# Optimization experiments

Measured on AMD Instinct MI355X. Metric: run time of the kernel, lower is better.

Reference implementation:

```python
import jax, jax.numpy as jnp
import numpy as np

INV_SQRT2 = 0.7071067811865476  # Haar (db1) lowpass on a length-1 zero-padded signal: cA = x/sqrt(2)


def setup_inputs() -> dict:
    key = jax.random.key(0)
    k = jax.random.split(key, 6)
    batch, node, dim = 4, 512, 64
    x = jax.random.normal(k[0], (batch, node, dim), dtype=jnp.float32)
    w0 = jax.random.normal(k[1], (1, 1), dtype=jnp.float32)   # linear[0].weight (always index 0 in source)
    b0 = jax.random.normal(k[2], (1,), dtype=jnp.float32)     # linear[0].bias
    wa = jax.random.normal(k[3], (dim,), dtype=jnp.float32)   # stacked attn_fc[i].weight (each 1x1)
    ba = jax.random.normal(k[4], (dim,), dtype=jnp.float32)   # stacked attn_fc[i].bias
    adj = jax.random.randint(k[5], (node, node), 0, 2, dtype=jnp.int32)
    return {"x": x, "w0": w0, "b0": b0, "wa": wa, "ba": ba, "adj": adj}


def reference(x, w0, b0, wa, ba, adj):
    # x: (b, n, d). Per-channel wavelet feature: softplus(linear0(cA)), cA = x/sqrt(2).
    feat = jax.nn.softplus(x * (INV_SQRT2 * w0[0, 0]) + b0[0])          # (b, n, d)
    scores = feat * wa + ba                                              # (b, n, d): attn_fc[i] per channel
    mask = adj > 0                                                       # (n, n)
    # attn_matrix[b,i,j,d] = scores[b,j,d] * mask[i,j], then masked-fill -1e9 where mask==0
    logits = scores[:, None, :, :] * mask[None, :, :, None].astype(scores.dtype)
    logits = jnp.where(mask[None, :, :, None], logits, jnp.float32(-1e9))
    attn = jax.nn.softmax(logits, axis=2)                                # softmax over j (neighbors)
    out = jnp.einsum('bijd,bjd->bid', attn, feat)                        # (b, n, d)
    return out
```

## Files before the change

kernel.cpp:

```cpp
#include <hip/hip_runtime.h>

#define NODE 512
#define DIM 64
#define BATCH 4

typedef __attribute__((ext_vector_type(8))) short bf16x8;
typedef __attribute__((ext_vector_type(4))) float f32x4;

#define LSTRIDE 520

__device__ __forceinline__ unsigned short f2bf(float f) {
    unsigned int u = __float_as_uint(f);
    u += 0x7FFF + ((u >> 16) & 1);
    return (unsigned short)(u >> 16);
}

__global__ __launch_bounds__(512) void k_fused3(const float* __restrict__ x,
                                                const float* __restrict__ w0,
                                                const float* __restrict__ b0,
                                                const float* __restrict__ wa,
                                                const float* __restrict__ ba,
                                                const int* __restrict__ adj,
                                                float* __restrict__ out) {
    __shared__ unsigned short Ep[16][LSTRIDE];
    __shared__ unsigned short Wp[16][LSTRIDE];
    __shared__ f32x4 red[2][4][2][64];

    const int blk = blockIdx.x;
    const int dt  = blk & 3;
    const int itg = (blk >> 2) & 15;
    const int b   = blk >> 6;
    const int tid = threadIdx.x;
    const int i0  = itg * 32;
    const int d0  = dt * 16;

    const int lane = tid & 63;
    const int w    = tid >> 6;
    const int itl  = w & 1;
    const int kq   = w >> 1;
    const int fr   = lane & 15;
    const int kg   = lane >> 4;

    const int* pAdj = adj + (i0 + itl * 16 + fr) * NODE + kq * 128 + kg * 8;
    int4 pa0[4], pa1[4];
    #pragma unroll
    for (int m = 0; m < 4; ++m) {
        pa0[m] = *(const int4*)(pAdj + m * 32);
        pa1[m] = *(const int4*)(pAdj + m * 32 + 4);
    }

    {
        const float c  = 0.7071067811865476f * w0[0];
        const float bb = b0[0];
        #pragma unroll
        for (int iter = 0; iter < 2; ++iter) {
            const int task = iter * 512 + tid;
            const int dg = task & 3;
            const int jp = task >> 2;
            const float* px = x + ((size_t)(b * NODE + 2 * jp) * DIM) + d0 + dg * 4;
            const float4 x0 = *(const float4*)px;
            const float4 x1 = *(const float4*)(px + DIM);
            #pragma unroll
            for (int i = 0; i < 4; ++i) {
                const int dl = dg * 4 + i;
                const float xv0 = (i == 0) ? x0.x : (i == 1) ? x0.y : (i == 2) ? x0.z : x0.w;
                const float xv1 = (i == 0) ? x1.x : (i == 1) ? x1.y : (i == 2) ? x1.z : x1.w;
                const float wad = wa[d0 + dl], bad = ba[d0 + dl];
                float z0 = fmaf(xv0, c, bb), z1 = fmaf(xv1, c, bb);
                float f0 = fmaxf(z0, 0.f) + __logf(1.f + __expf(-fabsf(z0)));
                float f1 = fmaxf(z1, 0.f) + __logf(1.f + __expf(-fabsf(z1)));
                float e0 = __expf(fmaf(f0, wad, bad));
                float e1 = __expf(fmaf(f1, wad, bad));
                unsigned int epk = (unsigned int)f2bf(e0) | ((unsigned int)f2bf(e1) << 16);
                unsigned int wpk = (unsigned int)f2bf(e0 * f0) | ((unsigned int)f2bf(e1 * f1) << 16);
                *(unsigned int*)&Ep[dl][2 * jp] = epk;
                *(unsigned int*)&Wp[dl][2 * jp] = wpk;
            }
        }
    }
    __syncthreads();

    const int jb0 = kq * 128 + kg * 8;
    f32x4 accD = {0.f, 0.f, 0.f, 0.f};
    f32x4 accN = {0.f, 0.f, 0.f, 0.f};
    #pragma unroll
    for (int m = 0; m < 4; ++m) {
        union { bf16x8 v; unsigned short s[8]; } A;
        A.s[0] = pa0[m].x ? 0x3F80 : 0;  A.s[1] = pa0[m].y ? 0x3F80 : 0;
        A.s[2] = pa0[m].z ? 0x3F80 : 0;  A.s[3] = pa0[m].w ? 0x3F80 : 0;
        A.s[4] = pa1[m].x ? 0x3F80 : 0;  A.s[5] = pa1[m].y ? 0x3F80 : 0;
        A.s[6] = pa1[m].z ? 0x3F80 : 0;  A.s[7] = pa1[m].w ? 0x3F80 : 0;
        const int jb = jb0 + m * 32;
        bf16x8 BD = *(const bf16x8*)&Ep[fr][jb];
        bf16x8 BN = *(const bf16x8*)&Wp[fr][jb];
        accD = __builtin_amdgcn_mfma_f32_16x16x32_bf16(A.v, BD, accD, 0, 0, 0);
        accN = __builtin_amdgcn_mfma_f32_16x16x32_bf16(A.v, BN, accN, 0, 0, 0);
    }

    red[itl][kq][0][lane] = accD;
    red[itl][kq][1][lane] = accN;
    __syncthreads();

    if (w < 2) {
        const int t = w;
        f32x4 D = red[t][0][0][lane] + red[t][1][0][lane] + red[t][2][0][lane] + red[t][3][0][lane];
        f32x4 N = red[t][0][1][lane] + red[t][1][1][lane] + red[t][2][1][lane] + red[t][3][1][lane];
        #pragma unroll
        for (int r = 0; r < 4; ++r) {
            float dd = D[r], nn = N[r];
            float o = (dd != 0.f) ? nn / dd : 0.f;
            out[((b * NODE) + i0 + t * 16 + kg * 4 + r) * DIM + d0 + fr] = o;
        }
    }
}

extern "C" void kernel_launch(void* const* d_in, const int* in_sizes, int n_in,
                              void* d_out, int out_size, void* d_ws, size_t ws_size,
                              hipStream_t stream) {
    const float* x  = (const float*)d_in[0];
    const float* w0 = (const float*)d_in[1];
    const float* b0 = (const float*)d_in[2];
    const float* wa = (const float*)d_in[3];
    const float* ba = (const float*)d_in[4];
    const int*  adj = (const int*)d_in[5];
    float* out = (float*)d_out;

    k_fused3<<<dim3(256), dim3(512), 0, stream>>>(x, w0, b0, wa, ba, adj, out);
}
```

Before: 9.895 us.

## Halve rows per block to 16 and split K over 8 waves, doubling grid

Each block now handles 16 output rows instead of 32, with all 8 waves splitting the 512-neighbor dimension into 64-wide chunks, and the grid grows from 256 to 512 blocks. This spreads work across more CUs on the GPU and shortens each wave's adjacency load and MFMA chain. All x loads are also issued up front before the softplus/exp work. The cost is that every block recomputes the full 512x16 exp/feature tables, so total transcendental work doubles, and the final reduction sums 8 partials in a single wave.

Result: slower. 10.86 us (+9.8%).

```diff
diff --git a/kernel.cpp b/kernel.cpp
--- a/kernel.cpp
+++ b/kernel.cpp
@@ -15,7 +15,7 @@
     return (unsigned short)(u >> 16);
 }
 
-__global__ __launch_bounds__(512) void k_fused3(const float* __restrict__ x,
+__global__ __launch_bounds__(512) void k_fused4(const float* __restrict__ x,
                                                 const float* __restrict__ w0,
                                                 const float* __restrict__ b0,
                                                 const float* __restrict__ wa,
@@ -24,47 +24,54 @@
                                                 float* __restrict__ out) {
     __shared__ unsigned short Ep[16][LSTRIDE];
     __shared__ unsigned short Wp[16][LSTRIDE];
-    __shared__ f32x4 red[2][4][2][64];
+    __shared__ f32x4 red[8][2][64];
 
     const int blk = blockIdx.x;
     const int dt  = blk & 3;
-    const int itg = (blk >> 2) & 15;
-    const int b   = blk >> 6;
+    const int it  = (blk >> 2) & 31;
+    const int b   = blk >> 7;
     const int tid = threadIdx.x;
-    const int i0  = itg * 32;
+    const int i0  = it * 16;
     const int d0  = dt * 16;
 
     const int lane = tid & 63;
     const int w    = tid >> 6;
-    const int itl  = w & 1;
-    const int kq   = w >> 1;
     const int fr   = lane & 15;
     const int kg   = lane >> 4;
 
-    const int* pAdj = adj + (i0 + itl * 16 + fr) * NODE + kq * 128 + kg * 8;
-    int4 pa0[4], pa1[4];
+    const int* pAdj = adj + (i0 + fr) * NODE + w * 64 + kg * 8;
+    int4 pa0[2], pa1[2];
     #pragma unroll
-    for (int m = 0; m < 4; ++m) {
+    for (int m = 0; m < 2; ++m) {
         pa0[m] = *(const int4*)(pAdj + m * 32);
         pa1[m] = *(const int4*)(pAdj + m * 32 + 4);
     }
 
     {
+        const int task0 = tid;
+        const int task1 = 512 + tid;
+        const int dgA = task0 & 3, jpA = task0 >> 2;
+        const int dgB = task1 & 3, jpB = task1 >> 2;
+        const float* pxA = x + ((size_t)(b * NODE + 2 * jpA) * DIM) + d0 + dgA * 4;
+        const float* pxB = x + ((size_t)(b * NODE + 2 * jpB) * DIM) + d0 + dgB * 4;
+        const float4 xA0 = *(const float4*)pxA;
+        const float4 xA1 = *(const float4*)(pxA + DIM);
+        const float4 xB0 = *(const float4*)pxB;
+        const float4 xB1 = *(const float4*)(pxB + DIM);
         const float c  = 0.7071067811865476f * w0[0];
         const float bb = b0[0];
+
         #pragma unroll
-        for (int iter = 0; iter < 2; ++iter) {
-            const int task = iter * 512 + tid;
-            const int dg = task & 3;
-            const int jp = task >> 2;
-            const float* px = x + ((size_t)(b * NODE + 2 * jp) * DIM) + d0 + dg * 4;
-            const float4 x0 = *(const float4*)px;
-            const float4 x1 = *(const float4*)(px + DIM);
+        for (int hh = 0; hh < 2; ++hh) {
+            const int dg = hh ? dgB : dgA;
+            const int jp = hh ? jpB : jpA;
+            const float4 v0 = hh ? xB0 : xA0;
+            const float4 v1 = hh ? xB1 : xA1;
             #pragma unroll
             for (int i = 0; i < 4; ++i) {
                 const int dl = dg * 4 + i;
-                const float xv0 = (i == 0) ? x0.x : (i == 1) ? x0.y : (i == 2) ? x0.z : x0.w;
-                const float xv1 = (i == 0) ? x1.x : (i == 1) ? x1.y : (i == 2) ? x1.z : x1.w;
+                const float xv0 = (i == 0) ? v0.x : (i == 1) ? v0.y : (i == 2) ? v0.z : v0.w;
+                const float xv1 = (i == 0) ? v1.x : (i == 1) ? v1.y : (i == 2) ? v1.z : v1.w;
                 const float wad = wa[d0 + dl], bad = ba[d0 + dl];
                 float z0 = fmaf(xv0, c, bb), z1 = fmaf(xv1, c, bb);
                 float f0 = fmaxf(z0, 0.f) + __logf(1.f + __expf(-fabsf(z0)));
@@ -80,11 +87,11 @@
     }
     __syncthreads();
 
-    const int jb0 = kq * 128 + kg * 8;
+    const int jb0 = w * 64 + kg * 8;
     f32x4 accD = {0.f, 0.f, 0.f, 0.f};
     f32x4 accN = {0.f, 0.f, 0.f, 0.f};
     #pragma unroll
-    for (int m = 0; m < 4; ++m) {
+    for (int m = 0; m < 2; ++m) {
         union { bf16x8 v; unsigned short s[8]; } A;
         A.s[0] = pa0[m].x ? 0x3F80 : 0;  A.s[1] = pa0[m].y ? 0x3F80 : 0;
         A.s[2] = pa0[m].z ? 0x3F80 : 0;  A.s[3] = pa0[m].w ? 0x3F80 : 0;
@@ -97,19 +104,23 @@
         accN = __builtin_amdgcn_mfma_f32_16x16x32_bf16(A.v, BN, accN, 0, 0, 0);
     }
 
-    red[itl][kq][0][lane] = accD;
-    red[itl][kq][1][lane] = accN;
+    red[w][0][lane] = accD;
+    red[w][1][lane] = accN;
     __syncthreads();
 
-    if (w < 2) {
-        const int t = w;
-        f32x4 D = red[t][0][0][lane] + red[t][1][0][lane] + red[t][2][0][lane] + red[t][3][0][lane];
-        f32x4 N = red[t][0][1][lane] + red[t][1][1][lane] + red[t][2][1][lane] + red[t][3][1][lane];
+    if (w == 0) {
+        f32x4 D = red[0][0][lane];
+        f32x4 N = red[0][1][lane];
+        #pragma unroll
+        for (int q = 1; q < 8; ++q) {
+            D += red[q][0][lane];
+            N += red[q][1][lane];
+        }
         #pragma unroll
         for (int r = 0; r < 4; ++r) {
             float dd = D[r], nn = N[r];
             float o = (dd != 0.f) ? nn / dd : 0.f;
-            out[((b * NODE) + i0 + t * 16 + kg * 4 + r) * DIM + d0 + fr] = o;
+            out[((b * NODE) + i0 + kg * 4 + r) * DIM + d0 + fr] = o;
         }
     }
 }
@@ -125,5 +136,5 @@
     const int*  adj = (const int*)d_in[5];
     float* out = (float*)d_out;
 
-    k_fused3<<<dim3(256), dim3(512), 0, stream>>>(x, w0, b0, wa, ba, adj, out);
+    k_fused4<<<dim3(512), dim3(512), 0, stream>>>(x, w0, b0, wa, ba, adj, out);
 }
```

## Retile blocks to 16 rows by 32 channels with XCD-aware mapping

Applied to the files above, without the earlier changes.

Each block now handles 16 output rows and 32 channels instead of 32 rows and 16 channels. The adjacency fragment loaded per wave is reused across two channel tiles, which halves adjacency reads per output. The softplus/exp precompute per block doubles, since it covers 32 channels. Block indices are remapped so consecutive row tiles land on the same XCD for L2 locality, and all x loads are hoisted ahead of the math to expose memory-level parallelism. The 8 waves split the reduction axis eight ways, so the final LDS reduction sums 8 partials instead of 4.

Measured after the change: 13.41 us. 1.35x slower.

```diff
diff --git a/kernel.cpp b/kernel.cpp
--- a/kernel.cpp
+++ b/kernel.cpp
@@ -15,58 +15,67 @@
     return (unsigned short)(u >> 16);
 }
 
-__global__ __launch_bounds__(512) void k_fused3(const float* __restrict__ x,
+__global__ __launch_bounds__(512) void k_fused5(const float* __restrict__ x,
                                                 const float* __restrict__ w0,
                                                 const float* __restrict__ b0,
                                                 const float* __restrict__ wa,
                                                 const float* __restrict__ ba,
                                                 const int* __restrict__ adj,
                                                 float* __restrict__ out) {
-    __shared__ unsigned short Ep[16][LSTRIDE];
-    __shared__ unsigned short Wp[16][LSTRIDE];
-    __shared__ f32x4 red[2][4][2][64];
+    __shared__ unsigned short Ep[32][LSTRIDE];
+    __shared__ unsigned short Wp[32][LSTRIDE];
+    __shared__ f32x4 red[8][2][2][64];
 
-    const int blk = blockIdx.x;
-    const int dt  = blk & 3;
-    const int itg = (blk >> 2) & 15;
-    const int b   = blk >> 6;
-    const int tid = threadIdx.x;
-    const int i0  = itg * 32;
-    const int d0  = dt * 16;
+    const int blk  = blockIdx.x;
+    const int xcd  = blk & 7;
+    const int rest = blk >> 3;
+    const int it   = xcd * 4 + (rest & 3);
+    const int dt2  = (rest >> 2) & 1;
+    const int b    = rest >> 3;
+    const int i0   = it * 16;
+    const int d0   = dt2 * 32;
 
+    const int tid  = threadIdx.x;
     const int lane = tid & 63;
     const int w    = tid >> 6;
-    const int itl  = w & 1;
-    const int kq   = w >> 1;
     const int fr   = lane & 15;
     const int kg   = lane >> 4;
 
-    const int* pAdj = adj + (i0 + itl * 16 + fr) * NODE + kq * 128 + kg * 8;
-    int4 pa0[4], pa1[4];
+    const int* pAdj = adj + (i0 + fr) * NODE + w * 64 + kg * 8;
+    int4 pa0[2], pa1[2];
     #pragma unroll
-    for (int m = 0; m < 4; ++m) {
+    for (int m = 0; m < 2; ++m) {
         pa0[m] = *(const int4*)(pAdj + m * 32);
         pa1[m] = *(const int4*)(pAdj + m * 32 + 4);
     }
 
+    float4 xv0[4], xv1[4];
+    #pragma unroll
+    for (int iter = 0; iter < 4; ++iter) {
+        const int task = iter * 512 + tid;
+        const int dg = task & 7;
+        const int jp = task >> 3;
+        const float* px = x + ((size_t)(b * NODE + 2 * jp) * DIM) + d0 + dg * 4;
+        xv0[iter] = *(const float4*)px;
+        xv1[iter] = *(const float4*)(px + DIM);
+    }
     {
         const float c  = 0.7071067811865476f * w0[0];
         const float bb = b0[0];
         #pragma unroll
-        for (int iter = 0; iter < 2; ++iter) {
+        for (int iter = 0; iter < 4; ++iter) {
             const int task = iter * 512 + tid;
-            const int dg = task & 3;
-            const int jp = task >> 2;
-            const float* px = x + ((size_t)(b * NODE + 2 * jp) * DIM) + d0 + dg * 4;
-            const float4 x0 = *(const float4*)px;
-            const float4 x1 = *(const float4*)(px + DIM);
+            const int dg = task & 7;
+            const int jp = task >> 3;
             #pragma unroll
             for (int i = 0; i < 4; ++i) {
                 const int dl = dg * 4 + i;
-                const float xv0 = (i == 0) ? x0.x : (i == 1) ? x0.y : (i == 2) ? x0.z : x0.w;
-                const float xv1 = (i == 0) ? x1.x : (i == 1) ? x1.y : (i == 2) ? x1.z : x1.w;
+                const float a0 = (i == 0) ? xv0[iter].x : (i == 1) ? xv0[iter].y
+                               : (i == 2) ? xv0[iter].z : xv0[iter].w;
+                const float a1 = (i == 0) ? xv1[iter].x : (i == 1) ? xv1[iter].y
+                               : (i == 2) ? xv1[iter].z : xv1[iter].w;
                 const float wad = wa[d0 + dl], bad = ba[d0 + dl];
-                float z0 = fmaf(xv0, c, bb), z1 = fmaf(xv1, c, bb);
+                float z0 = fmaf(a0, c, bb), z1 = fmaf(a1, c, bb);
                 float f0 = fmaxf(z0, 0.f) + __logf(1.f + __expf(-fabsf(z0)));
                 float f1 = fmaxf(z1, 0.f) + __logf(1.f + __expf(-fabsf(z1)));
                 float e0 = __expf(fmaf(f0, wad, bad));
@@ -80,36 +89,46 @@
     }
     __syncthreads();
 
-    const int jb0 = kq * 128 + kg * 8;
-    f32x4 accD = {0.f, 0.f, 0.f, 0.f};
-    f32x4 accN = {0.f, 0.f, 0.f, 0.f};
+    f32x4 accD[2] = {{0.f,0.f,0.f,0.f}, {0.f,0.f,0.f,0.f}};
+    f32x4 accN[2] = {{0.f,0.f,0.f,0.f}, {0.f,0.f,0.f,0.f}};
     #pragma unroll
-    for (int m = 0; m < 4; ++m) {
+    for (int m = 0; m < 2; ++m) {
         union { bf16x8 v; unsigned short s[8]; } A;
         A.s[0] = pa0[m].x ? 0x3F80 : 0;  A.s[1] = pa0[m].y ? 0x3F80 : 0;
         A.s[2] = pa0[m].z ? 0x3F80 : 0;  A.s[3] = pa0[m].w ? 0x3F80 : 0;
         A.s[4] = pa1[m].x ? 0x3F80 : 0;  A.s[5] = pa1[m].y ? 0x3F80 : 0;
         A.s[6] = pa1[m].z ? 0x3F80 : 0;  A.s[7] = pa1[m].w ? 0x3F80 : 0;
-        const int jb = jb0 + m * 32;
-        bf16x8 BD = *(const bf16x8*)&Ep[fr][jb];
-        bf16x8 BN = *(const bf16x8*)&Wp[fr][jb];
-        accD = __builtin_amdgcn_mfma_f32_16x16x32_bf16(A.v, BD, accD, 0, 0, 0);
-        accN = __builtin_amdgcn_mfma_f32_16x16x32_bf16(A.v, BN, accN, 0, 0, 0);
+        const int jb = w * 64 + m * 32 + kg * 8;
+        #pragma unroll
+        for (int dtl = 0; dtl < 2; ++dtl) {
+            bf16x8 BD = *(const bf16x8*)&Ep[dtl * 16 + fr][jb];
+            bf16x8 BN = *(const bf16x8*)&Wp[dtl * 16 + fr][jb];
+            accD[dtl] = __builtin_amdgcn_mfma_f32_16x16x32_bf16(A.v, BD, accD[dtl], 0, 0, 0);
+            accN[dtl] = __builtin_amdgcn_mfma_f32_16x16x32_bf16(A.v, BN, accN[dtl], 0, 0, 0);
+        }
     }
 
-    red[itl][kq][0][lane] = accD;
-    red[itl][kq][1][lane] = accN;
+    #pragma unroll
+    for (int dtl = 0; dtl < 2; ++dtl) {
+        red[w][dtl][0][lane] = accD[dtl];
+        red[w][dtl][1][lane] = accN[dtl];
+    }
     __syncthreads();
 
     if (w < 2) {
-        const int t = w;
-        f32x4 D = red[t][0][0][lane] + red[t][1][0][lane] + red[t][2][0][lane] + red[t][3][0][lane];
-        f32x4 N = red[t][0][1][lane] + red[t][1][1][lane] + red[t][2][1][lane] + red[t][3][1][lane];
+        const int dtl = w;
+        f32x4 D = red[0][dtl][0][lane];
+        f32x4 N = red[0][dtl][1][lane];
+        #pragma unroll
+        for (int q = 1; q < 8; ++q) {
+            D += red[q][dtl][0][lane];
+            N += red[q][dtl][1][lane];
+        }
         #pragma unroll
         for (int r = 0; r < 4; ++r) {
             float dd = D[r], nn = N[r];
             float o = (dd != 0.f) ? nn / dd : 0.f;
-            out[((b * NODE) + i0 + t * 16 + kg * 4 + r) * DIM + d0 + fr] = o;
+            out[((b * NODE) + i0 + kg * 4 + r) * DIM + d0 + dtl * 16 + fr] = o;
         }
     }
 }
@@ -125,5 +144,5 @@
     const int*  adj = (const int*)d_in[5];
     float* out = (float*)d_out;
 
-    k_fused3<<<dim3(256), dim3(512), 0, stream>>>(x, w0, b0, wa, ba, adj, out);
+    k_fused5<<<dim3(256), dim3(512), 0, stream>>>(x, w0, b0, wa, ba, adj, out);
 }
```
